# Performance work log

Measured on AMD Instinct MI355X. Metric: run time of the kernel, lower is better.

Reference implementation:

```python
import jax, jax.numpy as jnp
import numpy as np

B, S, D = 8, 1024, 1024
H, DK, DV = 16, 64, 64
EPS = 1e-5


def gaussian_prior(n_heads, len_q, len_k):
    # per-head causal Gaussian bias: exp(-(i-j)^2 / (2*sigma_h^2)) for i>=j else 0
    i = jnp.arange(len_q)[:, None]
    j = jnp.arange(len_k)[None, :]
    dist2 = (i - j).astype(jnp.float32) ** 2              # [S, S]
    sigma = jnp.arange(1, n_heads + 1, dtype=jnp.float32) # sigma_h = h+1
    bias = jnp.exp(-dist2[None] / (2.0 * sigma[:, None, None] ** 2))  # [H, S, S]
    return jnp.where(i >= j, bias, 0.0)


def setup_inputs() -> dict:
    key = jax.random.key(0)
    ks = jax.random.split(key, 7)
    input_Q = jax.random.normal(ks[0], (B, S, D), dtype=jnp.float32)
    input_K = jax.random.normal(ks[1], (B, S, D), dtype=jnp.float32)
    input_V = jax.random.normal(ks[2], (B, S, D), dtype=jnp.float32)
    # causal mask: True where attention is disallowed (j > i)
    causal = jnp.triu(jnp.ones((S, S), dtype=bool), k=1)
    attn_mask = jnp.broadcast_to(causal, (B, S, S))
    scale = 0.02
    Wq = jax.random.normal(ks[3], (H * DK, D), dtype=jnp.float32) * scale  # torch Linear weight [out,in]
    Wk = jax.random.normal(ks[4], (H * DK, D), dtype=jnp.float32) * scale
    Wv = jax.random.normal(ks[5], (H * DV, D), dtype=jnp.float32) * scale
    Wfc = jax.random.normal(ks[6], (D, H * DV), dtype=jnp.float32) * scale
    return {"input_Q": input_Q, "input_K": input_K, "input_V": input_V,
            "attn_mask": attn_mask, "Wq": Wq, "Wk": Wk, "Wv": Wv, "Wfc": Wfc}


def reference(input_Q, input_K, input_V, attn_mask, Wq, Wk, Wv, Wfc):
    b, s, d = input_Q.shape
    residual = input_Q
    # projections -> [B, H, S, dk]
    Q = (input_Q @ Wq.T).reshape(b, s, H, DK).transpose(0, 2, 1, 3)
    K = (input_K @ Wk.T).reshape(b, s, H, DK).transpose(0, 2, 1, 3)
    V = (input_V @ Wv.T).reshape(b, s, H, DV).transpose(0, 2, 1, 3)
    scores = jnp.einsum("bhqd,bhkd->bhqk", Q, K) / jnp.sqrt(jnp.float32(DK))
    scores = scores + gaussian_prior(H, s, s)[None]        # add Gaussian positional bias
    scores = jnp.where(attn_mask[:, None], -1e9, scores)   # masked_fill_
    attn = jax.nn.softmax(scores, axis=-1)
    context = jnp.einsum("bhqk,bhkd->bhqd", attn, V)
    context = context.transpose(0, 2, 1, 3).reshape(b, s, H * DV)
    output = context @ Wfc.T
    x = output + residual
    # LayerNorm (fresh module each call in source -> weight=1, bias=0)
    mu = jnp.mean(x, axis=-1, keepdims=True)
    var = jnp.var(x, axis=-1, keepdims=True)
    out = (x - mu) * jax.lax.rsqrt(var + EPS)
    return out, attn
```

## Files before the change

### kernel.cpp

```cpp
#include <hip/hip_runtime.h>
#include <hip/hip_bf16.h>

#define NP 8388608

typedef __attribute__((ext_vector_type(8))) short short8;
typedef __attribute__((ext_vector_type(4))) float f32x4;

__device__ __forceinline__ ushort f2bf(float f) {
  union { float f; unsigned u; } v; v.f = f;
  unsigned r = v.u + 0x7fffu + ((v.u >> 16) & 1u);
  return (ushort)(r >> 16);
}

__device__ __forceinline__ void gload16(const void* g, void* l) {
  __builtin_amdgcn_global_load_lds((const __attribute__((address_space(1))) void*)g,
                                   (__attribute__((address_space(3))) void*)l, 16, 0, 0);
}

__global__ void cast_inputs(const float* __restrict__ a, const float* __restrict__ b,
                            const float* __restrict__ c, ushort* __restrict__ dst) {
  const float* src = (blockIdx.y == 0) ? a : (blockIdx.y == 1) ? b : c;
  ushort* d = dst + (size_t)blockIdx.y * NP;
  size_t i = ((size_t)blockIdx.x * 256 + threadIdx.x) * 4;
  f32x4 v = *(const f32x4*)(src + i);
  ushort4 o; o.x = f2bf(v[0]); o.y = f2bf(v[1]); o.z = f2bf(v[2]); o.w = f2bf(v[3]);
  *(ushort4*)(d + i) = o;
}

__global__ void cast_weights(const float* __restrict__ w0, const float* __restrict__ w1,
                             const float* __restrict__ w2, const float* __restrict__ w3,
                             ushort* __restrict__ dst) {
  const float* src = (blockIdx.y == 0) ? w0 : (blockIdx.y == 1) ? w1
                    : (blockIdx.y == 2) ? w2 : w3;
  ushort* d = dst + (size_t)blockIdx.y * 1048576;
  size_t i = ((size_t)blockIdx.x * 256 + threadIdx.x) * 4;
  f32x4 v = *(const f32x4*)(src + i);
  ushort4 o; o.x = f2bf(v[0]); o.y = f2bf(v[1]); o.z = f2bf(v[2]); o.w = f2bf(v[3]);
  *(ushort4*)(d + i) = o;
}

template<int EPI>
__global__ __launch_bounds__(256) void gemm_bt(const ushort* __restrict__ Abase,
                                               const ushort* __restrict__ Bbase,
                                               float* __restrict__ Cf32,
                                               ushort* __restrict__ Qh,
                                               ushort* __restrict__ Kh,
                                               ushort* __restrict__ VhT) {
  constexpr int K = 1024;
  __shared__ ushort As[8192];
  __shared__ ushort Bs[8192];
  const int t = threadIdx.x, w = t >> 6, l = t & 63;
  const int o  = blockIdx.y * 8 + blockIdx.x;
  const int o2 = (o & 7) * 64 + (o >> 3);
  const int n0 = (o2 & 7) * 128, m0 = (o2 >> 3) * 128;
  const int z = blockIdx.z;
  const ushort* A  = Abase + (EPI == 0 ? (size_t)z * NP : 0);
  const ushort* Bm = Bbase + (EPI == 0 ? (size_t)z * 1048576 : 0);

  f32x4 acc[4][4];
#pragma unroll
  for (int i = 0; i < 4; i++)
#pragma unroll
    for (int j = 0; j < 4; j++) acc[i][j] = f32x4{0.f, 0.f, 0.f, 0.f};

  const int wm = w >> 1, wn = w & 1;
  const int srow = w * 8 + (l >> 3);
  const int sc = l & 7;
  const int fr = l & 15, fq = l >> 4;
  const int fswz = fr & 7;

  for (int k0 = 0; k0 < K; k0 += 64) {
    __syncthreads();
#pragma unroll
    for (int r = 0; r < 4; r++) {
      int row = r * 32 + srow;
      int col = (sc ^ (row & 7)) * 8;
      gload16(A  + (size_t)(m0 + row) * K + k0 + col, &As[r * 2048 + w * 512]);
      gload16(Bm + (size_t)(n0 + row) * K + k0 + col, &Bs[r * 2048 + w * 512]);
    }
    __syncthreads();
#pragma unroll
    for (int s2 = 0; s2 < 2; s2++) {
      short8 av[4], bv[4];
      const int ck = ((s2 * 4 + fq) ^ fswz) * 8;
#pragma unroll
      for (int i = 0; i < 4; i++) {
        av[i] = *(const short8*)&As[(wm * 64 + i * 16 + fr) * 64 + ck];
        bv[i] = *(const short8*)&Bs[(wn * 64 + i * 16 + fr) * 64 + ck];
      }
#pragma unroll
      for (int i = 0; i < 4; i++)
#pragma unroll
        for (int j = 0; j < 4; j++)
          acc[i][j] = __builtin_amdgcn_mfma_f32_16x16x32_bf16(bv[j], av[i], acc[i][j], 0, 0, 0);
    }
  }

#pragma unroll
  for (int i = 0; i < 4; i++) {
    int m = m0 + wm * 64 + i * 16 + fr;
#pragma unroll
    for (int j = 0; j < 4; j++) {
      int n = n0 + wn * 64 + j * 16 + fq * 4;
      f32x4 v = acc[i][j];
      if (EPI == 1) {
        *(f32x4*)(Cf32 + (size_t)m * 1024 + n) = v;
      } else {
        int b = m >> 10, s = m & 1023, h = n >> 6, d = n & 63;
        if (z == 0) {
          ushort4 q; q.x = f2bf(v[0] * 0.125f); q.y = f2bf(v[1] * 0.125f);
          q.z = f2bf(v[2] * 0.125f); q.w = f2bf(v[3] * 0.125f);
          *(ushort4*)(Qh + ((size_t)(b * 16 + h) * 1024 + s) * 64 + d) = q;
        } else if (z == 1) {
          ushort4 q; q.x = f2bf(v[0]); q.y = f2bf(v[1]);
          q.z = f2bf(v[2]); q.w = f2bf(v[3]);
          *(ushort4*)(Kh + ((size_t)(b * 16 + h) * 1024 + s) * 64 + d) = q;
        } else {
#pragma unroll
          for (int reg = 0; reg < 4; reg++)
            VhT[((size_t)(b * 16 + h) * 64 + d + reg) * 1024 + s] = f2bf(v[reg]);
        }
      }
    }
  }
}

__global__ __launch_bounds__(256) void attn_fused(const ushort* __restrict__ Qh,
                                                  const ushort* __restrict__ Kh,
                                                  const ushort* __restrict__ VhT,
                                                  float* __restrict__ attnO,
                                                  ushort* __restrict__ ctx) {
  __shared__ ushort Kt[2][4096];
  __shared__ ushort Vt[4096];
  __shared__ ushort Pl[4096];
  __shared__ float  biasl[1024];

  const int t = threadIdx.x, w = t >> 6, l = t & 63;
  const int o = blockIdx.x + 8 * blockIdx.y + 128 * blockIdx.z;
  const int gx = (o >> 3) & 7;
  const int bhid = (o & 7) + 8 * (o >> 6);
  const int h = bhid & 15, b = bhid >> 4;
  const size_t bh = (size_t)b * 16 + h;
  const int fr = l & 15, fq = l >> 4, fk = fq * 8;

  const float sig = (float)(h + 1);
  const float minv = -1.0f / (2.0f * sig * sig);
  for (int d = t; d < 1024; d += 256) {
    float fd = (float)d;
    biasl[d] = __expf(fd * fd * minv);
  }

  const int srow = w * 8 + (l >> 3);
  const int sc = l & 7;
  char* Prow = (char*)(Pl + w * 1024 + fr * 64);
  const int pswz = (fr & 7) << 4;

  auto stageK = [&](int kt, int bsel) {
#pragma unroll
    for (int r = 0; r < 2; r++) {
      int row = r * 32 + srow;
      int col = (sc ^ (row & 7)) * 8;
      gload16(Kh + (bh * 1024 + kt * 64 + row) * 64 + col, &Kt[bsel][r * 2048 + w * 512]);
    }
  };
  auto stageV = [&](int kt) {
#pragma unroll
    for (int r = 0; r < 2; r++) {
      int row = r * 32 + srow;
      int col = (sc ^ (row & 7)) * 8;
      gload16(VhT + (bh * 64 + row) * 1024 + kt * 64 + col, &Vt[r * 2048 + w * 512]);
    }
  };

  for (int half = 0; half < 2; half++) {
    const int qt = half ? 15 - gx : gx;
    const int q0 = qt * 64;
    const int qrow_g = q0 + w * 16 + fr;

    const ushort* qrow = Qh + (bh * 1024 + qrow_g) * 64;
    short8 qa0 = *(const short8*)(qrow + fk);
    short8 qa1 = *(const short8*)(qrow + 32 + fk);

    float psum = 0.f;
    stageK(0, 0);
    asm volatile("s_waitcnt vmcnt(0) lgkmcnt(0)" ::: "memory");
    __builtin_amdgcn_s_barrier();
    for (int kt = 0; kt <= qt; kt++) {
      const int cur = kt & 1;
      if (kt < qt) stageK(kt + 1, cur ^ 1);
      __builtin_amdgcn_sched_barrier(0);
#pragma unroll
      for (int cb = 0; cb < 4; cb++) {
        int krow = cb * 16 + fr;
        short8 kb0 = *(const short8*)&Kt[cur][krow * 64 + ((fq ^ (krow & 7)) * 8)];
        short8 kb1 = *(const short8*)&Kt[cur][krow * 64 + (((fq + 4) ^ (krow & 7)) * 8)];
        f32x4 s = f32x4{0.f, 0.f, 0.f, 0.f};
        __builtin_amdgcn_s_setprio(1);
        s = __builtin_amdgcn_mfma_f32_16x16x32_bf16(kb0, qa0, s, 0, 0, 0);
        s = __builtin_amdgcn_mfma_f32_16x16x32_bf16(kb1, qa1, s, 0, 0, 0);
        __builtin_amdgcn_s_setprio(0);
        int kbase = kt * 64 + cb * 16 + fq * 4;
#pragma unroll
        for (int reg = 0; reg < 4; reg++) {
          int dd = qrow_g - (kbase + reg);
          float bb = biasl[max(dd, 0)];
          float p = __expf(s[reg] + bb);
          if (dd >= 0) psum += p;
        }
      }
      asm volatile("s_waitcnt vmcnt(0)" ::: "memory");
      __builtin_amdgcn_s_barrier();
    }
    psum += __shfl_xor(psum, 16, 64);
    psum += __shfl_xor(psum, 32, 64);
    const float linv = 1.0f / psum;

    f32x4 cacc[4];
#pragma unroll
    for (int nb = 0; nb < 4; nb++) cacc[nb] = f32x4{0.f, 0.f, 0.f, 0.f};

    float* arow_p = attnO + (bh * 1024 + qrow_g) * 1024;

    stageK(0, 0);
    asm volatile("s_waitcnt vmcnt(0)" ::: "memory");
    __builtin_amdgcn_s_barrier();
    for (int kt = 0; kt <= qt; kt++) {
      const int cur = kt & 1;
      stageV(kt);
      if (kt < qt) stageK(kt + 1, cur ^ 1);
      __builtin_amdgcn_sched_barrier(0);

#pragma unroll
      for (int cb = 0; cb < 4; cb++) {
        int krow = cb * 16 + fr;
        short8 kb0 = *(const short8*)&Kt[cur][krow * 64 + ((fq ^ (krow & 7)) * 8)];
        short8 kb1 = *(const short8*)&Kt[cur][krow * 64 + (((fq + 4) ^ (krow & 7)) * 8)];
        f32x4 s = f32x4{0.f, 0.f, 0.f, 0.f};
        __builtin_amdgcn_s_setprio(1);
        s = __builtin_amdgcn_mfma_f32_16x16x32_bf16(kb0, qa0, s, 0, 0, 0);
        s = __builtin_amdgcn_mfma_f32_16x16x32_bf16(kb1, qa1, s, 0, 0, 0);
        __builtin_amdgcn_s_setprio(0);
        int kbase = kt * 64 + cb * 16 + fq * 4;
        f32x4 o;
#pragma unroll
        for (int reg = 0; reg < 4; reg++) {
          int dd = qrow_g - (kbase + reg);
          float bb = biasl[max(dd, 0)];
          float p = __expf(s[reg] + bb) * linv;
          o[reg] = (dd >= 0) ? p : 0.0f;
        }
        *(f32x4*)(arow_p + kbase) = o;
        uint2 pk;
        asm("v_cvt_pk_bf16_f32 %0, %1, %2" : "=v"(pk.x) : "v"(o[0]), "v"(o[1]));
        asm("v_cvt_pk_bf16_f32 %0, %1, %2" : "=v"(pk.y) : "v"(o[2]), "v"(o[3]));
        *(uint2*)(Prow + (((cb * 32 + fq * 8) ^ pswz))) = pk;
      }

      if (kt < qt) { asm volatile("s_waitcnt vmcnt(6) lgkmcnt(0)" ::: "memory"); }
      else         { asm volatile("s_waitcnt vmcnt(4) lgkmcnt(0)" ::: "memory"); }
      __builtin_amdgcn_s_barrier();
      __builtin_amdgcn_sched_barrier(0);

      short8 pa0 = *(const short8*)(Prow + ((fq * 16) ^ pswz));
      short8 pa1 = *(const short8*)(Prow + ((64 + fq * 16) ^ pswz));
      __builtin_amdgcn_s_setprio(1);
#pragma unroll
      for (int nb = 0; nb < 4; nb++) {
        int vrow = nb * 16 + fr;
        short8 vb0 = *(const short8*)&Vt[vrow * 64 + ((fq ^ (vrow & 7)) * 8)];
        short8 vb1 = *(const short8*)&Vt[vrow * 64 + (((fq + 4) ^ (vrow & 7)) * 8)];
        cacc[nb] = __builtin_amdgcn_mfma_f32_16x16x32_bf16(pa0, vb0, cacc[nb], 0, 0, 0);
        cacc[nb] = __builtin_amdgcn_mfma_f32_16x16x32_bf16(pa1, vb1, cacc[nb], 0, 0, 0);
      }
      __builtin_amdgcn_s_setprio(0);

      asm volatile("s_waitcnt vmcnt(4)" ::: "memory");
      __builtin_amdgcn_s_barrier();
    }

    int cstart = (qt + 1) * 64;
    if (cstart < 1024) {
      int W4 = (1024 - cstart) >> 2;
      for (int r = w; r < 64; r += 4) {
        float* dst = attnO + (bh * 1024 + q0 + r) * 1024 + cstart;
        for (int c = l; c < W4; c += 64)
          __builtin_nontemporal_store(f32x4{0.f, 0.f, 0.f, 0.f}, (f32x4*)dst + c);
      }
    }

#pragma unroll
    for (int nb = 0; nb < 4; nb++)
#pragma unroll
      for (int reg = 0; reg < 4; reg++) {
        int s = q0 + w * 16 + fq * 4 + reg;
        int col = h * 64 + nb * 16 + fr;
        ctx[((size_t)b * 1024 + s) * 1024 + col] = f2bf(cacc[nb][reg]);
      }
  }
}

__global__ __launch_bounds__(256) void ln_kernel(const float* __restrict__ fc,
                                                 const float* __restrict__ resid,
                                                 float* __restrict__ out) {
  const int row = blockIdx.x, t = threadIdx.x, w = t >> 6, l = t & 63;
  f32x4 xf = *(const f32x4*)(fc    + (size_t)row * 1024 + t * 4);
  f32x4 xr = *(const f32x4*)(resid + (size_t)row * 1024 + t * 4);
  f32x4 x;
#pragma unroll
  for (int i = 0; i < 4; i++) x[i] = xf[i] + xr[i];
  float s1 = x[0] + x[1] + x[2] + x[3];
  float s2 = x[0]*x[0] + x[1]*x[1] + x[2]*x[2] + x[3]*x[3];
#pragma unroll
  for (int off = 1; off < 64; off <<= 1) {
    s1 += __shfl_xor(s1, off, 64);
    s2 += __shfl_xor(s2, off, 64);
  }
  __shared__ float red[8];
  if (l == 0) { red[w] = s1; red[4 + w] = s2; }
  __syncthreads();
  float S1 = red[0] + red[1] + red[2] + red[3];
  float S2 = red[4] + red[5] + red[6] + red[7];
  float mu = S1 * (1.0f / 1024.0f);
  float var = S2 * (1.0f / 1024.0f) - mu * mu;
  float rs = rsqrtf(var + 1e-5f);
  f32x4 o;
#pragma unroll
  for (int i = 0; i < 4; i++) o[i] = (x[i] - mu) * rs;
  *(f32x4*)(out + (size_t)row * 1024 + t * 4) = o;
}

extern "C" void kernel_launch(void* const* d_in, const int* in_sizes, int n_in,
                              void* d_out, int out_size, void* d_ws, size_t ws_size,
                              hipStream_t stream) {
  const float* inQ = (const float*)d_in[0];
  const float* inK = (const float*)d_in[1];
  const float* inV = (const float*)d_in[2];
  const float* Wq  = (const float*)d_in[4];
  const float* Wk  = (const float*)d_in[5];
  const float* Wv  = (const float*)d_in[6];
  const float* Wfc = (const float*)d_in[7];
  float* out   = (float*)d_out;
  float* attnO = out + (size_t)NP;

  char* wsb = (char*)d_ws;
  ushort* Wb   = (ushort*)wsb;
  ushort* inXb = (ushort*)(wsb + 8388608ull);
  ushort* Qh   = (ushort*)(wsb + 58720256ull);
  ushort* Kh   = (ushort*)(wsb + 75497472ull);
  ushort* VhT  = (ushort*)(wsb + 92274688ull);
  ushort* ctx  = (ushort*)(wsb + 8388608ull);
  float*  fcO  = (float*)(wsb + 25165824ull);

  cast_inputs <<<dim3(8192, 3), 256, 0, stream>>>(inQ, inK, inV, inXb);
  cast_weights<<<dim3(1024, 4), 256, 0, stream>>>(Wq, Wk, Wv, Wfc, Wb);
  gemm_bt<0>  <<<dim3(8, 64, 3), 256, 0, stream>>>(inXb, Wb, nullptr, Qh, Kh, VhT);
  attn_fused  <<<dim3(8, 16, 8), 256, 0, stream>>>(Qh, Kh, VhT, attnO, ctx);
  gemm_bt<1>  <<<dim3(8, 64, 1), 256, 0, stream>>>(ctx, Wb + 3145728, fcO,
                                                   nullptr, nullptr, nullptr);
  ln_kernel   <<<8192, 256, 0, stream>>>(fcO, inQ, out);
}
```

Before: 276.2 us.

## Read K and V fragments directly from global memory instead of LDS staging

Removes the double-buffered LDS staging of K and V tiles, along with the barriers and waitcnt choreography around it. Each wave now loads its MFMA operand fragments straight from global memory through the cache. This frees LDS and drops block-level synchronization. The cost is redundant global and L2 traffic, since all four waves now fetch the same K and V rows independently, and load latency is no longer overlapped by an explicit prefetch.

Result: slower. 369.3 us (+33.7%).

```diff
diff --git a/kernel.cpp b/kernel.cpp
--- a/kernel.cpp
+++ b/kernel.cpp
@@ -130,8 +130,6 @@
                                                   const ushort* __restrict__ VhT,
                                                   float* __restrict__ attnO,
                                                   ushort* __restrict__ ctx) {
-  __shared__ ushort Kt[2][4096];
-  __shared__ ushort Vt[4096];
   __shared__ ushort Pl[4096];
   __shared__ float  biasl[1024];
 
@@ -149,28 +147,12 @@
     float fd = (float)d;
     biasl[d] = __expf(fd * fd * minv);
   }
-
-  const int srow = w * 8 + (l >> 3);
-  const int sc = l & 7;
+  __syncthreads();
+
+  const ushort* Kbh = Kh  + bh * 65536;
+  const ushort* Vbh = VhT + bh * 65536;
   char* Prow = (char*)(Pl + w * 1024 + fr * 64);
   const int pswz = (fr & 7) << 4;
-
-  auto stageK = [&](int kt, int bsel) {
-#pragma unroll
-    for (int r = 0; r < 2; r++) {
-      int row = r * 32 + srow;
-      int col = (sc ^ (row & 7)) * 8;
-      gload16(Kh + (bh * 1024 + kt * 64 + row) * 64 + col, &Kt[bsel][r * 2048 + w * 512]);
-    }
-  };
-  auto stageV = [&](int kt) {
-#pragma unroll
-    for (int r = 0; r < 2; r++) {
-      int row = r * 32 + srow;
-      int col = (sc ^ (row & 7)) * 8;
-      gload16(VhT + (bh * 64 + row) * 1024 + kt * 64 + col, &Vt[r * 2048 + w * 512]);
-    }
-  };
 
   for (int half = 0; half < 2; half++) {
     const int qt = half ? 15 - gx : gx;
@@ -182,18 +164,12 @@
     short8 qa1 = *(const short8*)(qrow + 32 + fk);
 
     float psum = 0.f;
-    stageK(0, 0);
-    asm volatile("s_waitcnt vmcnt(0) lgkmcnt(0)" ::: "memory");
-    __builtin_amdgcn_s_barrier();
     for (int kt = 0; kt <= qt; kt++) {
-      const int cur = kt & 1;
-      if (kt < qt) stageK(kt + 1, cur ^ 1);
-      __builtin_amdgcn_sched_barrier(0);
 #pragma unroll
       for (int cb = 0; cb < 4; cb++) {
-        int krow = cb * 16 + fr;
-        short8 kb0 = *(const short8*)&Kt[cur][krow * 64 + ((fq ^ (krow & 7)) * 8)];
-        short8 kb1 = *(const short8*)&Kt[cur][krow * 64 + (((fq + 4) ^ (krow & 7)) * 8)];
+        const ushort* kp = Kbh + (size_t)(kt * 64 + cb * 16 + fr) * 64;
+        short8 kb0 = *(const short8*)(kp + fk);
+        short8 kb1 = *(const short8*)(kp + 32 + fk);
         f32x4 s = f32x4{0.f, 0.f, 0.f, 0.f};
         __builtin_amdgcn_s_setprio(1);
         s = __builtin_amdgcn_mfma_f32_16x16x32_bf16(kb0, qa0, s, 0, 0, 0);
@@ -208,8 +184,6 @@
           if (dd >= 0) psum += p;
         }
       }
-      asm volatile("s_waitcnt vmcnt(0)" ::: "memory");
-      __builtin_amdgcn_s_barrier();
     }
     psum += __shfl_xor(psum, 16, 64);
     psum += __shfl_xor(psum, 32, 64);
@@ -221,44 +195,34 @@
 
     float* arow_p = attnO + (bh * 1024 + qrow_g) * 1024;
 
-    stageK(0, 0);
-    asm volatile("s_waitcnt vmcnt(0)" ::: "memory");
-    __builtin_amdgcn_s_barrier();
     for (int kt = 0; kt <= qt; kt++) {
-      const int cur = kt & 1;
-      stageV(kt);
-      if (kt < qt) stageK(kt + 1, cur ^ 1);
-      __builtin_amdgcn_sched_barrier(0);
-
 #pragma unroll
       for (int cb = 0; cb < 4; cb++) {
-        int krow = cb * 16 + fr;
-        short8 kb0 = *(const short8*)&Kt[cur][krow * 64 + ((fq ^ (krow & 7)) * 8)];
-        short8 kb1 = *(const short8*)&Kt[cur][krow * 64 + (((fq + 4) ^ (krow & 7)) * 8)];
+        const ushort* kp = Kbh + (size_t)(kt * 64 + cb * 16 + fr) * 64;
+        short8 kb0 = *(const short8*)(kp + fk);
+        short8 kb1 = *(const short8*)(kp + 32 + fk);
         f32x4 s = f32x4{0.f, 0.f, 0.f, 0.f};
         __builtin_amdgcn_s_setprio(1);
         s = __builtin_amdgcn_mfma_f32_16x16x32_bf16(kb0, qa0, s, 0, 0, 0);
         s = __builtin_amdgcn_mfma_f32_16x16x32_bf16(kb1, qa1, s, 0, 0, 0);
         __builtin_amdgcn_s_setprio(0);
         int kbase = kt * 64 + cb * 16 + fq * 4;
-        f32x4 o;
+        f32x4 oo;
 #pragma unroll
         for (int reg = 0; reg < 4; reg++) {
           int dd = qrow_g - (kbase + reg);
           float bb = biasl[max(dd, 0)];
           float p = __expf(s[reg] + bb) * linv;
-          o[reg] = (dd >= 0) ? p : 0.0f;
+          oo[reg] = (dd >= 0) ? p : 0.0f;
         }
-        *(f32x4*)(arow_p + kbase) = o;
+        *(f32x4*)(arow_p + kbase) = oo;
         uint2 pk;
-        asm("v_cvt_pk_bf16_f32 %0, %1, %2" : "=v"(pk.x) : "v"(o[0]), "v"(o[1]));
-        asm("v_cvt_pk_bf16_f32 %0, %1, %2" : "=v"(pk.y) : "v"(o[2]), "v"(o[3]));
+        asm("v_cvt_pk_bf16_f32 %0, %1, %2" : "=v"(pk.x) : "v"(oo[0]), "v"(oo[1]));
+        asm("v_cvt_pk_bf16_f32 %0, %1, %2" : "=v"(pk.y) : "v"(oo[2]), "v"(oo[3]));
         *(uint2*)(Prow + (((cb * 32 + fq * 8) ^ pswz))) = pk;
       }
 
-      if (kt < qt) { asm volatile("s_waitcnt vmcnt(6) lgkmcnt(0)" ::: "memory"); }
-      else         { asm volatile("s_waitcnt vmcnt(4) lgkmcnt(0)" ::: "memory"); }
-      __builtin_amdgcn_s_barrier();
+      asm volatile("s_waitcnt lgkmcnt(0)" ::: "memory");
       __builtin_amdgcn_sched_barrier(0);
 
       short8 pa0 = *(const short8*)(Prow + ((fq * 16) ^ pswz));
@@ -266,16 +230,13 @@
       __builtin_amdgcn_s_setprio(1);
 #pragma unroll
       for (int nb = 0; nb < 4; nb++) {
-        int vrow = nb * 16 + fr;
-        short8 vb0 = *(const short8*)&Vt[vrow * 64 + ((fq ^ (vrow & 7)) * 8)];
-        short8 vb1 = *(const short8*)&Vt[vrow * 64 + (((fq + 4) ^ (vrow & 7)) * 8)];
+        const ushort* vp = Vbh + (size_t)(nb * 16 + fr) * 1024 + kt * 64;
+        short8 vb0 = *(const short8*)(vp + fk);
+        short8 vb1 = *(const short8*)(vp + 32 + fk);
         cacc[nb] = __builtin_amdgcn_mfma_f32_16x16x32_bf16(pa0, vb0, cacc[nb], 0, 0, 0);
         cacc[nb] = __builtin_amdgcn_mfma_f32_16x16x32_bf16(pa1, vb1, cacc[nb], 0, 0, 0);
       }
       __builtin_amdgcn_s_setprio(0);
-
-      asm volatile("s_waitcnt vmcnt(4)" ::: "memory");
-      __builtin_amdgcn_s_barrier();
     }
 
     int cstart = (qt + 1) * 64;
```

## Share K tiles across both query tiles in pass 1, fuse residual into FC GEMM

Applied to the files above, without the earlier changes.

In the attention kernel's first pass, which computes softmax denominators, both paired query tiles (gx and 15-gx) are now processed in one sweep over K. Each K tile is loaded into LDS once instead of twice, and the number of barriers is roughly halved. The second pass is split into a lambda that runs for each tile in turn. Separately, the residual add moves into the FC GEMM epilogue so LayerNorm reads one fp32 tensor instead of two, and the attention-probability stores become nontemporal. This costs more live registers for the second set of Q fragments and the extra psum.

New measurement: 306.8 us. 1.11x slower.

```diff
diff --git a/kernel.cpp b/kernel.cpp
--- a/kernel.cpp
+++ b/kernel.cpp
@@ -45,7 +45,8 @@
                                                float* __restrict__ Cf32,
                                                ushort* __restrict__ Qh,
                                                ushort* __restrict__ Kh,
-                                               ushort* __restrict__ VhT) {
+                                               ushort* __restrict__ VhT,
+                                               const float* __restrict__ Resid) {
   constexpr int K = 1024;
   __shared__ ushort As[8192];
   __shared__ ushort Bs[8192];
@@ -104,6 +105,9 @@
       int n = n0 + wn * 64 + j * 16 + fq * 4;
       f32x4 v = acc[i][j];
       if (EPI == 1) {
+        f32x4 rr = *(const f32x4*)(Resid + (size_t)m * 1024 + n);
+#pragma unroll
+        for (int reg = 0; reg < 4; reg++) v[reg] += rr[reg];
         *(f32x4*)(Cf32 + (size_t)m * 1024 + n) = v;
       } else {
         int b = m >> 10, s = m & 1023, h = n >> 6, d = n & 63;
@@ -172,23 +176,86 @@
     }
   };
 
-  for (int half = 0; half < 2; half++) {
-    const int qt = half ? 15 - gx : gx;
-    const int q0 = qt * 64;
-    const int qrow_g = q0 + w * 16 + fr;
-
-    const ushort* qrow = Qh + (bh * 1024 + qrow_g) * 64;
-    short8 qa0 = *(const short8*)(qrow + fk);
-    short8 qa1 = *(const short8*)(qrow + 32 + fk);
-
-    float psum = 0.f;
+  const int qtA = gx, qtB = 15 - gx;
+  const int qrowA = qtA * 64 + w * 16 + fr;
+  const int qrowB = qtB * 64 + w * 16 + fr;
+
+  const ushort* qpA = Qh + (bh * 1024 + qrowA) * 64;
+  const ushort* qpB = Qh + (bh * 1024 + qrowB) * 64;
+  short8 qaA0 = *(const short8*)(qpA + fk);
+  short8 qaA1 = *(const short8*)(qpA + 32 + fk);
+  short8 qaB0 = *(const short8*)(qpB + fk);
+  short8 qaB1 = *(const short8*)(qpB + 32 + fk);
+
+  float psumA = 0.f, psumB = 0.f;
+  stageK(0, 0);
+  asm volatile("s_waitcnt vmcnt(0) lgkmcnt(0)" ::: "memory");
+  __builtin_amdgcn_s_barrier();
+  for (int kt = 0; kt <= qtB; kt++) {
+    const int cur = kt & 1;
+    if (kt < qtB) stageK(kt + 1, cur ^ 1);
+    __builtin_amdgcn_sched_barrier(0);
+#pragma unroll
+    for (int cb = 0; cb < 4; cb++) {
+      int krow = cb * 16 + fr;
+      short8 kb0 = *(const short8*)&Kt[cur][krow * 64 + ((fq ^ (krow & 7)) * 8)];
+      short8 kb1 = *(const short8*)&Kt[cur][krow * 64 + (((fq + 4) ^ (krow & 7)) * 8)];
+      int kbase = kt * 64 + cb * 16 + fq * 4;
+      {
+        f32x4 s = f32x4{0.f, 0.f, 0.f, 0.f};
+        __builtin_amdgcn_s_setprio(1);
+        s = __builtin_amdgcn_mfma_f32_16x16x32_bf16(kb0, qaB0, s, 0, 0, 0);
+        s = __builtin_amdgcn_mfma_f32_16x16x32_bf16(kb1, qaB1, s, 0, 0, 0);
+        __builtin_amdgcn_s_setprio(0);
+#pragma unroll
+        for (int reg = 0; reg < 4; reg++) {
+          int dd = qrowB - (kbase + reg);
+          float bb = biasl[max(dd, 0)];
+          float p = __expf(s[reg] + bb);
+          if (dd >= 0) psumB += p;
+        }
+      }
+      if (kt <= qtA) {
+        f32x4 s = f32x4{0.f, 0.f, 0.f, 0.f};
+        __builtin_amdgcn_s_setprio(1);
+        s = __builtin_amdgcn_mfma_f32_16x16x32_bf16(kb0, qaA0, s, 0, 0, 0);
+        s = __builtin_amdgcn_mfma_f32_16x16x32_bf16(kb1, qaA1, s, 0, 0, 0);
+        __builtin_amdgcn_s_setprio(0);
+#pragma unroll
+        for (int reg = 0; reg < 4; reg++) {
+          int dd = qrowA - (kbase + reg);
+          float bb = biasl[max(dd, 0)];
+          float p = __expf(s[reg] + bb);
+          if (dd >= 0) psumA += p;
+        }
+      }
+    }
+    asm volatile("s_waitcnt vmcnt(0)" ::: "memory");
+    __builtin_amdgcn_s_barrier();
+  }
+  psumA += __shfl_xor(psumA, 16, 64);
+  psumA += __shfl_xor(psumA, 32, 64);
+  psumB += __shfl_xor(psumB, 16, 64);
+  psumB += __shfl_xor(psumB, 32, 64);
+  const float linvA = 1.0f / psumA;
+  const float linvB = 1.0f / psumB;
+
+  auto pass2 = [&](int qt, int qrow_g, short8 qa0, short8 qa1, float linv) {
+    f32x4 cacc[4];
+#pragma unroll
+    for (int nb = 0; nb < 4; nb++) cacc[nb] = f32x4{0.f, 0.f, 0.f, 0.f};
+
+    float* arow_p = attnO + (bh * 1024 + qrow_g) * 1024;
+
     stageK(0, 0);
-    asm volatile("s_waitcnt vmcnt(0) lgkmcnt(0)" ::: "memory");
+    asm volatile("s_waitcnt vmcnt(0)" ::: "memory");
     __builtin_amdgcn_s_barrier();
     for (int kt = 0; kt <= qt; kt++) {
       const int cur = kt & 1;
+      stageV(kt);
       if (kt < qt) stageK(kt + 1, cur ^ 1);
       __builtin_amdgcn_sched_barrier(0);
+
 #pragma unroll
       for (int cb = 0; cb < 4; cb++) {
         int krow = cb * 16 + fr;
@@ -200,59 +267,18 @@
         s = __builtin_amdgcn_mfma_f32_16x16x32_bf16(kb1, qa1, s, 0, 0, 0);
         __builtin_amdgcn_s_setprio(0);
         int kbase = kt * 64 + cb * 16 + fq * 4;
-#pragma unroll
-        for (int reg = 0; reg < 4; reg++) {
-          int dd = qrow_g - (kbase + reg);
-          float bb = biasl[max(dd, 0)];
-          float p = __expf(s[reg] + bb);
-          if (dd >= 0) psum += p;
-        }
-      }
-      asm volatile("s_waitcnt vmcnt(0)" ::: "memory");
-      __builtin_amdgcn_s_barrier();
-    }
-    psum += __shfl_xor(psum, 16, 64);
-    psum += __shfl_xor(psum, 32, 64);
-    const float linv = 1.0f / psum;
-
-    f32x4 cacc[4];
-#pragma unroll
-    for (int nb = 0; nb < 4; nb++) cacc[nb] = f32x4{0.f, 0.f, 0.f, 0.f};
-
-    float* arow_p = attnO + (bh * 1024 + qrow_g) * 1024;
-
-    stageK(0, 0);
-    asm volatile("s_waitcnt vmcnt(0)" ::: "memory");
-    __builtin_amdgcn_s_barrier();
-    for (int kt = 0; kt <= qt; kt++) {
-      const int cur = kt & 1;
-      stageV(kt);
-      if (kt < qt) stageK(kt + 1, cur ^ 1);
-      __builtin_amdgcn_sched_barrier(0);
-
-#pragma unroll
-      for (int cb = 0; cb < 4; cb++) {
-        int krow = cb * 16 + fr;
-        short8 kb0 = *(const short8*)&Kt[cur][krow * 64 + ((fq ^ (krow & 7)) * 8)];
-        short8 kb1 = *(const short8*)&Kt[cur][krow * 64 + (((fq + 4) ^ (krow & 7)) * 8)];
-        f32x4 s = f32x4{0.f, 0.f, 0.f, 0.f};
-        __builtin_amdgcn_s_setprio(1);
-        s = __builtin_amdgcn_mfma_f32_16x16x32_bf16(kb0, qa0, s, 0, 0, 0);
-        s = __builtin_amdgcn_mfma_f32_16x16x32_bf16(kb1, qa1, s, 0, 0, 0);
-        __builtin_amdgcn_s_setprio(0);
-        int kbase = kt * 64 + cb * 16 + fq * 4;
-        f32x4 o;
+        f32x4 oo;
 #pragma unroll
         for (int reg = 0; reg < 4; reg++) {
           int dd = qrow_g - (kbase + reg);
           float bb = biasl[max(dd, 0)];
           float p = __expf(s[reg] + bb) * linv;
-          o[reg] = (dd >= 0) ? p : 0.0f;
+          oo[reg] = (dd >= 0) ? p : 0.0f;
         }
-        *(f32x4*)(arow_p + kbase) = o;
+        __builtin_nontemporal_store(oo, (f32x4*)(arow_p + kbase));
         uint2 pk;
-        asm("v_cvt_pk_bf16_f32 %0, %1, %2" : "=v"(pk.x) : "v"(o[0]), "v"(o[1]));
-        asm("v_cvt_pk_bf16_f32 %0, %1, %2" : "=v"(pk.y) : "v"(o[2]), "v"(o[3]));
+        asm("v_cvt_pk_bf16_f32 %0, %1, %2" : "=v"(pk.x) : "v"(oo[0]), "v"(oo[1]));
+        asm("v_cvt_pk_bf16_f32 %0, %1, %2" : "=v"(pk.y) : "v"(oo[2]), "v"(oo[3]));
         *(uint2*)(Prow + (((cb * 32 + fq * 8) ^ pswz))) = pk;
       }
 
@@ -278,6 +304,7 @@
       __builtin_amdgcn_s_barrier();
     }
 
+    int q0 = qt * 64;
     int cstart = (qt + 1) * 64;
     if (cstart < 1024) {
       int W4 = (1024 - cstart) >> 2;
@@ -296,18 +323,16 @@
         int col = h * 64 + nb * 16 + fr;
         ctx[((size_t)b * 1024 + s) * 1024 + col] = f2bf(cacc[nb][reg]);
       }
-  }
-}
-
-__global__ __launch_bounds__(256) void ln_kernel(const float* __restrict__ fc,
-                                                 const float* __restrict__ resid,
+  };
+
+  pass2(qtA, qrowA, qaA0, qaA1, linvA);
+  pass2(qtB, qrowB, qaB0, qaB1, linvB);
+}
+
+__global__ __launch_bounds__(256) void ln_kernel(const float* __restrict__ xin,
                                                  float* __restrict__ out) {
   const int row = blockIdx.x, t = threadIdx.x, w = t >> 6, l = t & 63;
-  f32x4 xf = *(const f32x4*)(fc    + (size_t)row * 1024 + t * 4);
-  f32x4 xr = *(const f32x4*)(resid + (size_t)row * 1024 + t * 4);
-  f32x4 x;
-#pragma unroll
-  for (int i = 0; i < 4; i++) x[i] = xf[i] + xr[i];
+  f32x4 x = *(const f32x4*)(xin + (size_t)row * 1024 + t * 4);
   float s1 = x[0] + x[1] + x[2] + x[3];
   float s2 = x[0]*x[0] + x[1]*x[1] + x[2]*x[2] + x[3]*x[3];
 #pragma unroll
@@ -353,9 +378,9 @@
 
   cast_inputs <<<dim3(8192, 3), 256, 0, stream>>>(inQ, inK, inV, inXb);
   cast_weights<<<dim3(1024, 4), 256, 0, stream>>>(Wq, Wk, Wv, Wfc, Wb);
-  gemm_bt<0>  <<<dim3(8, 64, 3), 256, 0, stream>>>(inXb, Wb, nullptr, Qh, Kh, VhT);
+  gemm_bt<0>  <<<dim3(8, 64, 3), 256, 0, stream>>>(inXb, Wb, nullptr, Qh, Kh, VhT, nullptr);
   attn_fused  <<<dim3(8, 16, 8), 256, 0, stream>>>(Qh, Kh, VhT, attnO, ctx);
   gemm_bt<1>  <<<dim3(8, 64, 1), 256, 0, stream>>>(ctx, Wb + 3145728, fcO,
-                                                   nullptr, nullptr, nullptr);
-  ln_kernel   <<<8192, 256, 0, stream>>>(fcO, inQ, out);
-}
+                                                   nullptr, nullptr, nullptr, inQ);
+  ln_kernel   <<<8192, 256, 0, stream>>>(fcO, out);
+}
```

## Skip Gaussian bias for far tiles and fuse residual add into FC GEMM

Applied to the files above, without the earlier changes.

In the attention kernel, key tiles that lie entirely more than about 4.5 sigma below the diagonal skip the bias lookup, the causal check and the mask select, and use plain exp of the score. This drops LDS bias reads and integer work from most tiles in both the row-sum pass and the output pass. It also moves the residual add into the output GEMM epilogue, so the LayerNorm kernel reads one tensor instead of two. The bias skipped is below exp(-10), so the effect on results is negligible but not exactly zero.

New measurement: 275.2 us. About the same (-0.4%).

```diff
diff --git a/kernel.cpp b/kernel.cpp
--- a/kernel.cpp
+++ b/kernel.cpp
@@ -45,7 +45,8 @@
                                                float* __restrict__ Cf32,
                                                ushort* __restrict__ Qh,
                                                ushort* __restrict__ Kh,
-                                               ushort* __restrict__ VhT) {
+                                               ushort* __restrict__ VhT,
+                                               const float* __restrict__ Resid) {
   constexpr int K = 1024;
   __shared__ ushort As[8192];
   __shared__ ushort Bs[8192];
@@ -104,6 +105,9 @@
       int n = n0 + wn * 64 + j * 16 + fq * 4;
       f32x4 v = acc[i][j];
       if (EPI == 1) {
+        f32x4 rr = *(const f32x4*)(Resid + (size_t)m * 1024 + n);
+#pragma unroll
+        for (int reg = 0; reg < 4; reg++) v[reg] += rr[reg];
         *(f32x4*)(Cf32 + (size_t)m * 1024 + n) = v;
       } else {
         int b = m >> 10, s = m & 1023, h = n >> 6, d = n & 63;
@@ -145,6 +149,7 @@
 
   const float sig = (float)(h + 1);
   const float minv = -1.0f / (2.0f * sig * sig);
+  const int bcut = (int)(4.5f * sig) + 1;
   for (int d = t; d < 1024; d += 256) {
     float fd = (float)d;
     biasl[d] = __expf(fd * fd * minv);
@@ -176,6 +181,7 @@
     const int qt = half ? 15 - gx : gx;
     const int q0 = qt * 64;
     const int qrow_g = q0 + w * 16 + fr;
+    const int wrow0 = q0 + w * 16;
 
     const ushort* qrow = Qh + (bh * 1024 + qrow_g) * 64;
     short8 qa0 = *(const short8*)(qrow + fk);
@@ -189,6 +195,54 @@
       const int cur = kt & 1;
       if (kt < qt) stageK(kt + 1, cur ^ 1);
       __builtin_amdgcn_sched_barrier(0);
+      const bool nobias = (wrow0 - kt * 64 - 63) > bcut;
+#pragma unroll
+      for (int cb = 0; cb < 4; cb++) {
+        int krow = cb * 16 + fr;
+        short8 kb0 = *(const short8*)&Kt[cur][krow * 64 + ((fq ^ (krow & 7)) * 8)];
+        short8 kb1 = *(const short8*)&Kt[cur][krow * 64 + (((fq + 4) ^ (krow & 7)) * 8)];
+        f32x4 s = f32x4{0.f, 0.f, 0.f, 0.f};
+        __builtin_amdgcn_s_setprio(1);
+        s = __builtin_amdgcn_mfma_f32_16x16x32_bf16(kb0, qa0, s, 0, 0, 0);
+        s = __builtin_amdgcn_mfma_f32_16x16x32_bf16(kb1, qa1, s, 0, 0, 0);
+        __builtin_amdgcn_s_setprio(0);
+        if (nobias) {
+#pragma unroll
+          for (int reg = 0; reg < 4; reg++) psum += __expf(s[reg]);
+        } else {
+          int kbase = kt * 64 + cb * 16 + fq * 4;
+#pragma unroll
+          for (int reg = 0; reg < 4; reg++) {
+            int dd = qrow_g - (kbase + reg);
+            float bb = biasl[max(dd, 0)];
+            float p = __expf(s[reg] + bb);
+            if (dd >= 0) psum += p;
+          }
+        }
+      }
+      asm volatile("s_waitcnt vmcnt(0)" ::: "memory");
+      __builtin_amdgcn_s_barrier();
+    }
+    psum += __shfl_xor(psum, 16, 64);
+    psum += __shfl_xor(psum, 32, 64);
+    const float linv = 1.0f / psum;
+
+    f32x4 cacc[4];
+#pragma unroll
+    for (int nb = 0; nb < 4; nb++) cacc[nb] = f32x4{0.f, 0.f, 0.f, 0.f};
+
+    float* arow_p = attnO + (bh * 1024 + qrow_g) * 1024;
+
+    stageK(0, 0);
+    asm volatile("s_waitcnt vmcnt(0)" ::: "memory");
+    __builtin_amdgcn_s_barrier();
+    for (int kt = 0; kt <= qt; kt++) {
+      const int cur = kt & 1;
+      stageV(kt);
+      if (kt < qt) stageK(kt + 1, cur ^ 1);
+      __builtin_amdgcn_sched_barrier(0);
+      const bool nobias = (wrow0 - kt * 64 - 63) > bcut;
+
 #pragma unroll
       for (int cb = 0; cb < 4; cb++) {
         int krow = cb * 16 + fr;
@@ -200,59 +254,23 @@
         s = __builtin_amdgcn_mfma_f32_16x16x32_bf16(kb1, qa1, s, 0, 0, 0);
         __builtin_amdgcn_s_setprio(0);
         int kbase = kt * 64 + cb * 16 + fq * 4;
-#pragma unroll
-        for (int reg = 0; reg < 4; reg++) {
-          int dd = qrow_g - (kbase + reg);
-          float bb = biasl[max(dd, 0)];
-          float p = __expf(s[reg] + bb);
-          if (dd >= 0) psum += p;
+        f32x4 oo;
+        if (nobias) {
+#pragma unroll
+          for (int reg = 0; reg < 4; reg++) oo[reg] = __expf(s[reg]) * linv;
+        } else {
+#pragma unroll
+          for (int reg = 0; reg < 4; reg++) {
+            int dd = qrow_g - (kbase + reg);
+            float bb = biasl[max(dd, 0)];
+            float p = __expf(s[reg] + bb) * linv;
+            oo[reg] = (dd >= 0) ? p : 0.0f;
+          }
         }
-      }
-      asm volatile("s_waitcnt vmcnt(0)" ::: "memory");
-      __builtin_amdgcn_s_barrier();
-    }
-    psum += __shfl_xor(psum, 16, 64);
-    psum += __shfl_xor(psum, 32, 64);
-    const float linv = 1.0f / psum;
-
-    f32x4 cacc[4];
-#pragma unroll
-    for (int nb = 0; nb < 4; nb++) cacc[nb] = f32x4{0.f, 0.f, 0.f, 0.f};
-
-    float* arow_p = attnO + (bh * 1024 + qrow_g) * 1024;
-
-    stageK(0, 0);
-    asm volatile("s_waitcnt vmcnt(0)" ::: "memory");
-    __builtin_amdgcn_s_barrier();
-    for (int kt = 0; kt <= qt; kt++) {
-      const int cur = kt & 1;
-      stageV(kt);
-      if (kt < qt) stageK(kt + 1, cur ^ 1);
-      __builtin_amdgcn_sched_barrier(0);
-
-#pragma unroll
-      for (int cb = 0; cb < 4; cb++) {
-        int krow = cb * 16 + fr;
-        short8 kb0 = *(const short8*)&Kt[cur][krow * 64 + ((fq ^ (krow & 7)) * 8)];
-        short8 kb1 = *(const short8*)&Kt[cur][krow * 64 + (((fq + 4) ^ (krow & 7)) * 8)];
-        f32x4 s = f32x4{0.f, 0.f, 0.f, 0.f};
-        __builtin_amdgcn_s_setprio(1);
-        s = __builtin_amdgcn_mfma_f32_16x16x32_bf16(kb0, qa0, s, 0, 0, 0);
-        s = __builtin_amdgcn_mfma_f32_16x16x32_bf16(kb1, qa1, s, 0, 0, 0);
-        __builtin_amdgcn_s_setprio(0);
-        int kbase = kt * 64 + cb * 16 + fq * 4;
-        f32x4 o;
-#pragma unroll
-        for (int reg = 0; reg < 4; reg++) {
-          int dd = qrow_g - (kbase + reg);
-          float bb = biasl[max(dd, 0)];
-          float p = __expf(s[reg] + bb) * linv;
-          o[reg] = (dd >= 0) ? p : 0.0f;
-        }
-        *(f32x4*)(arow_p + kbase) = o;
+        *(f32x4*)(arow_p + kbase) = oo;
         uint2 pk;
-        asm("v_cvt_pk_bf16_f32 %0, %1, %2" : "=v"(pk.x) : "v"(o[0]), "v"(o[1]));
-        asm("v_cvt_pk_bf16_f32 %0, %1, %2" : "=v"(pk.y) : "v"(o[2]), "v"(o[3]));
+        asm("v_cvt_pk_bf16_f32 %0, %1, %2" : "=v"(pk.x) : "v"(oo[0]), "v"(oo[1]));
+        asm("v_cvt_pk_bf16_f32 %0, %1, %2" : "=v"(pk.y) : "v"(oo[2]), "v"(oo[3]));
         *(uint2*)(Prow + (((cb * 32 + fq * 8) ^ pswz))) = pk;
       }
 
@@ -299,15 +317,10 @@
   }
 }
 
-__global__ __launch_bounds__(256) void ln_kernel(const float* __restrict__ fc,
-                                                 const float* __restrict__ resid,
+__global__ __launch_bounds__(256) void ln_kernel(const float* __restrict__ xin,
                                                  float* __restrict__ out) {
   const int row = blockIdx.x, t = threadIdx.x, w = t >> 6, l = t & 63;
-  f32x4 xf = *(const f32x4*)(fc    + (size_t)row * 1024 + t * 4);
-  f32x4 xr = *(const f32x4*)(resid + (size_t)row * 1024 + t * 4);
-  f32x4 x;
-#pragma unroll
-  for (int i = 0; i < 4; i++) x[i] = xf[i] + xr[i];
+  f32x4 x = *(const f32x4*)(xin + (size_t)row * 1024 + t * 4);
   float s1 = x[0] + x[1] + x[2] + x[3];
   float s2 = x[0]*x[0] + x[1]*x[1] + x[2]*x[2] + x[3]*x[3];
 #pragma unroll
@@ -353,9 +366,9 @@
 
   cast_inputs <<<dim3(8192, 3), 256, 0, stream>>>(inQ, inK, inV, inXb);
   cast_weights<<<dim3(1024, 4), 256, 0, stream>>>(Wq, Wk, Wv, Wfc, Wb);
-  gemm_bt<0>  <<<dim3(8, 64, 3), 256, 0, stream>>>(inXb, Wb, nullptr, Qh, Kh, VhT);
+  gemm_bt<0>  <<<dim3(8, 64, 3), 256, 0, stream>>>(inXb, Wb, nullptr, Qh, Kh, VhT, nullptr);
   attn_fused  <<<dim3(8, 16, 8), 256, 0, stream>>>(Qh, Kh, VhT, attnO, ctx);
   gemm_bt<1>  <<<dim3(8, 64, 1), 256, 0, stream>>>(ctx, Wb + 3145728, fcO,
-                                                   nullptr, nullptr, nullptr);
-  ln_kernel   <<<8192, 256, 0, stream>>>(fcO, inQ, out);
-}
+                                                   nullptr, nullptr, nullptr, inQ);
+  ln_kernel   <<<8192, 256, 0, stream>>>(fcO, out);
+}
```
